# Optimization experiments

Measured on AMD Instinct MI355X. Metric: run time of the kernel, lower is better.

## Reference

```python
import jax, jax.numpy as jnp
import numpy as np
from jax import lax

V = 100000       # vocab_size / num_words
E = 300          # embedding_size (== num_units, required by compare stage)
M = 300          # num_units / mem_dim
NC = 3           # num_classes
L = 128          # leaves per tree -> N = 2L-1 nodes
N = 2 * L - 1


def build_tree(num_leaves):
    # balanced binary tree, postorder node numbering (children before parent)
    left, right = [], []
    def rec(lo, hi):
        if hi - lo == 1:
            left.append(-1); right.append(-1)
            return len(left) - 1
        mid = (lo + hi) // 2
        l = rec(lo, mid)
        r = rec(mid, hi)
        left.append(l); right.append(r)
        return len(left) - 1
    rec(0, num_leaves)
    return np.asarray(left, np.int32), np.asarray(right, np.int32)


def setup_inputs() -> dict:
    key = jax.random.key(0)
    ks = jax.random.split(key, 20)
    l1, r1 = build_tree(L)
    l2, r2 = build_tree(L)
    s = 0.1  # param scale (stands in for orthogonal init)
    inp = {
        "sent1": jax.random.randint(ks[0], (N,), 0, V),
        "sent2": jax.random.randint(ks[1], (N,), 0, V),
        "left1": jnp.asarray(l1), "right1": jnp.asarray(r1),
        "left2": jnp.asarray(l2), "right2": jnp.asarray(r2),
        "emb": jax.random.normal(ks[2], (V, E), jnp.float32),
        # composer x-projections, gate order: [cx, ix, fx, ox]
        "Wx_i": jax.random.normal(ks[3], (4, M, E), jnp.float32) * s,
        "bx_i": jnp.zeros((4, M), jnp.float32),
        # composer h-projections, gate order: [u, i, lf, rf, o]
        "Wl_i": jax.random.normal(ks[4], (5, M, M), jnp.float32) * s,
        "Wr_i": jax.random.normal(ks[5], (5, M, M), jnp.float32) * s,
        "Wx_c": jax.random.normal(ks[6], (4, M, M), jnp.float32) * s,
        "bx_c": jnp.zeros((4, M), jnp.float32),
        "Wl_c": jax.random.normal(ks[7], (5, M, M), jnp.float32) * s,
        "Wr_c": jax.random.normal(ks[8], (5, M, M), jnp.float32) * s,
        "Wc": jax.random.normal(ks[9], (M, 4 * M), jnp.float32) * 0.01,
        "bc": jnp.zeros((M,), jnp.float32),
        "Wa1": jax.random.normal(ks[10], (M, 4 * M), jnp.float32) * 0.01,
        "ba1": jnp.zeros((M,), jnp.float32),
        "Wa2": jax.random.normal(ks[11], (NC, M), jnp.float32) * 0.01,
        "ba2": jnp.zeros((NC,), jnp.float32),
    }
    return inp


def tree_lstm(xg, left, right, Wl, Wr):
    # xg: [N, 4, M] precomputed x-gate terms (cx, ix, fx, ox)
    # Wl/Wr: [5, M, M] hidden-state gate weights (u, i, lf, rf, o)
    n, _, m = xg.shape
    zero = jnp.zeros((m,), xg.dtype)

    def step(carry, t):
        C, H = carry
        i, l, r = t
        lc = jnp.where(l >= 0, C[jnp.maximum(l, 0)], zero)
        lh = jnp.where(l >= 0, H[jnp.maximum(l, 0)], zero)
        rc = jnp.where(r >= 0, C[jnp.maximum(r, 0)], zero)
        rh = jnp.where(r >= 0, H[jnp.maximum(r, 0)], zero)
        gl = jnp.einsum('gmd,d->gm', Wl, lh)  # [5, M]
        gr = jnp.einsum('gmd,d->gm', Wr, rh)
        x = xg[i]  # [4, M]
        u  = jnp.tanh(x[0] + gl[0] + gr[0])
        ig = jax.nn.sigmoid(x[1] + gl[1] + gr[1])
        lf = jax.nn.sigmoid(x[2] + gl[2] + gr[2])  # fx shared for both forgets (as in source)
        rf = jax.nn.sigmoid(x[2] + gl[3] + gr[3])
        c = ig * u + lf * lc + rf * rc
        o = jax.nn.sigmoid(x[3] + gl[4] + gr[4])
        h = o * jnp.tanh(c)
        return (C.at[i].set(c), H.at[i].set(h)), None

    init = (jnp.zeros((n, m), xg.dtype), jnp.zeros((n, m), xg.dtype))
    (_, H), _ = lax.scan(step, init, (jnp.arange(n), left, right))
    return H  # [N, M] all node hidden states in postorder


def reference(sent1, sent2, left1, right1, left2, right2, emb,
              Wx_i, bx_i, Wl_i, Wr_i, Wx_c, bx_c, Wl_c, Wr_c,
              Wc, bc, Wa1, ba1, Wa2, ba2):
    pad = emb.shape[0] - 1  # num_words - 1

    def encode(sent, left, right):
        # leaves embed their token; internal nodes embed PAD (PAD=True path)
        tok = jnp.where(left < 0, sent, pad)
        x = emb[tok]                                        # [N, E]
        xg = jnp.einsum('nd,gmd->ngm', x, Wx_i) + bx_i      # [N, 4, M]
        return tree_lstm(xg, left, right, Wl_i, Wr_i)

    s1 = encode(sent1, left1, right1)  # [N1, M]
    s2 = encode(sent2, left2, right2)  # [N2, M]

    raw = s1 @ s2.T                                         # [N1, N2]
    beta = jax.nn.softmax(raw, axis=1) @ s2                 # aligned to s1
    alpha = jax.nn.softmax(raw.T, axis=1) @ s1              # aligned to s2

    def compare(s, a, left, right):
        feat = jnp.concatenate([s, a, s - a, s * a], axis=-1)  # [N, 4M]
        h = jax.nn.relu(feat @ Wc.T + bc)                      # [N, M]
        xg = jnp.einsum('nd,gmd->ngm', h, Wx_c) + bx_c
        return tree_lstm(xg, left, right, Wl_c, Wr_c)

    v1 = compare(s1, beta, left1, right1)
    v2 = compare(s2, alpha, left2, right2)

    agg = jnp.concatenate([v1.mean(0), v1.max(0), v2.mean(0), v2.max(0)])  # [4M]
    hidden = jax.nn.relu(agg @ Wa1.T + ba1)
    logits = hidden @ Wa2.T + ba2
    return logits[None, :]  # [1, num_classes]
```

## Files before the change

### kernel.cpp

```cpp
#include <hip/hip_runtime.h>
#include <math.h>

#define NN 255
#define TC 510
#define HTLD 512
#define RSH 5

typedef unsigned int uint32;

__device__ __forceinline__ float sigm(float x){ return 1.f/(1.f+expf(-x)); }

__device__ __forceinline__ float aload(const float* p){ return __hip_atomic_load(p, __ATOMIC_RELAXED, __HIP_MEMORY_SCOPE_AGENT); }
__device__ __forceinline__ void astore(float* p, float v){ __hip_atomic_store(p, v, __ATOMIC_RELAXED, __HIP_MEMORY_SCOPE_AGENT); }
__device__ __forceinline__ uint32 aloadu(const uint32* p){ return __hip_atomic_load(p, __ATOMIC_RELAXED, __HIP_MEMORY_SCOPE_AGENT); }

__device__ __forceinline__ void leaf_gate(const float* __restrict__ xgp, int m, float& c, float& h){
  float x0 = xgp[m], x1 = xgp[300+m], x3 = xgp[900+m];
  float u = tanhf(x0), ig = sigm(x1);
  c = ig * u;
  h = sigm(x3) * tanhf(c);
}

__global__ __launch_bounds__(512) void k_setup(const int* __restrict__ l1, const int* __restrict__ r1,
                                               const int* __restrict__ l2, const int* __restrict__ r2,
                                               int4* __restrict__ lists2, int* __restrict__ cnt)
{
  __shared__ int lv[TC];
  __shared__ int cs[16];
  int t = threadIdx.x;
  if (t < TC) lv[t] = 0;
  if (t < 16) cs[t] = 0;
  __syncthreads();
  for (int it = 0; it < 12; ++it){
    int nv = 0;
    if (t < TC){
      int tr = t >= NN, i = t - tr * NN;
      const int* L = tr ? l2 : l1;
      const int* R = tr ? r2 : r1;
      int l = L[i], r = R[i];
      nv = (l < 0) ? 0 : 1 + max(lv[tr * NN + l], lv[tr * NN + r]);
    }
    __syncthreads();
    if (t < TC) lv[t] = nv;
    __syncthreads();
  }
  if (t < TC){
    int tr = t >= NN, i = t - tr * NN;
    int v = min(lv[t], 15);
    int pos = atomicAdd(&cs[v], 1);
    int l = (tr ? l2 : l1)[i], r = (tr ? r2 : r1)[i];
    lists2[v * 256 + pos] = make_int4(tr * NN + i, tr * NN + max(l, 0), tr * NN + max(r, 0), 0);
  }
  __syncthreads();
  if (t < 16) cnt[t] = cs[t];
}

template<int NG>
__global__ __launch_bounds__(256, 3) void k_tree(
    const float* __restrict__ Wl, const float* __restrict__ Wr,
    const float* __restrict__ xg, int xrow,
    float* __restrict__ H, float* __restrict__ C, float* __restrict__ HT,
    const int4* __restrict__ lists2, const int* __restrict__ cnt,
    uint32* __restrict__ rdy)
{
  constexpr int NB = NG * 75;
  __shared__ float Hs[16][2][320];
  __shared__ float Cs[16][4][2];
  __shared__ float Xs[16][4][4];
  __shared__ int4 nfo[512];
  __shared__ int lvoff[9];

  const int tid = threadIdx.x;
  const int lane = tid & 63, team = tid >> 6;
  const int mblk = blockIdx.x % 75, grp = blockIdx.x / 75;
  const int m = mblk * 4 + team;

  float wl[5][5], wr[5][5];
  #pragma unroll
  for (int g = 0; g < 5; ++g)
    #pragma unroll
    for (int j = 0; j < 5; ++j){
      int d = j * 64 + lane;
      size_t o = ((size_t)g * 300 + m) * 300 + d;
      wl[g][j] = (d < 300) ? Wl[o] : 0.f;
      wr[g][j] = (d < 300) ? Wr[o] : 0.f;
    }

  if (tid == 0){ lvoff[0] = 0; for (int lv = 1; lv <= 7; ++lv) lvoff[lv] = lvoff[lv-1] + cnt[lv-1]; }
  __syncthreads();
  for (int lv = 0; lv <= 7; ++lv)
    for (int i = tid; i < cnt[lv]; i += 256)
      nfo[lvoff[lv] + i] = lists2[lv * 256 + i];
  __syncthreads();

  {
    int nodes = cnt[0];
    int npg = (nodes + NG - 1) / NG;
    int n0 = grp * npg, n1 = min(nodes, n0 + npg);
    for (int nb0 = n0; nb0 < n1; nb0 += 64){
      int nch = min(64, n1 - nb0);
      if (tid < nch * 4){
        int ni = tid >> 2, tm = tid & 3;
        int gi = nfo[nb0 + ni].x;
        int mm = mblk * 4 + tm;
        float c, h; leaf_gate(xg + (size_t)gi * 1200, mm, c, h);
        astore(&C[(size_t)gi * 300 + mm], c);
        astore(&H[(size_t)gi * 300 + mm], h);
        astore(&HT[(size_t)mm * HTLD + gi], h);
      }
      asm volatile("s_waitcnt vmcnt(0)" ::: "memory");
      __syncthreads();
      if (tid < nch) atomicAdd(&rdy[(uint32)nfo[nb0 + tid].x << RSH], 1u);
    }
  }

  for (int lv = 1; lv <= 7; ++lv){
    int nodes = cnt[lv];
    int npg = (nodes + NG - 1) / NG;
    int n0 = grp * npg, n1 = min(nodes, n0 + npg);
    for (int nb0 = n0; nb0 < n1; nb0 += 16){
      int nch = min(16, n1 - nb0);
      int base = lvoff[lv] + nb0;
      __syncthreads();
      if (tid < nch){
        int4 nn = nfo[base + tid];
        while (aloadu(&rdy[(uint32)nn.y << RSH]) < 75u) __builtin_amdgcn_s_sleep(4);
        while (aloadu(&rdy[(uint32)nn.z << RSH]) < 75u) __builtin_amdgcn_s_sleep(4);
      }
      __syncthreads();
      #pragma unroll
      for (int p = 0; p < 2; ++p){
        int niA = team + p * 8, niB = niA + 4;
        bool vA = niA < nch, vB = niB < nch;
        int4 na = vA ? nfo[base + niA] : make_int4(0, 0, 0, 0);
        int4 nb4 = vB ? nfo[base + niB] : make_int4(0, 0, 0, 0);
        int d0 = lane, d1 = 64 + lane, d2 = 128 + lane, d3 = 192 + lane, d4 = 256 + lane;
        bool i4 = d4 < 300;
        #define LDH(ci, dd, ok) ((ok) ? aload(&H[(size_t)(ci) * 300 + (dd)]) : 0.f)
        float a0=LDH(na.y,d0,vA), a1=LDH(na.y,d1,vA), a2=LDH(na.y,d2,vA), a3=LDH(na.y,d3,vA), a4=LDH(na.y,d4,vA&&i4);
        float a5=LDH(na.z,d0,vA), a6=LDH(na.z,d1,vA), a7=LDH(na.z,d2,vA), a8=LDH(na.z,d3,vA), a9=LDH(na.z,d4,vA&&i4);
        float c0=LDH(nb4.y,d0,vB), c1=LDH(nb4.y,d1,vB), c2=LDH(nb4.y,d2,vB), c3=LDH(nb4.y,d3,vB), c4=LDH(nb4.y,d4,vB&&i4);
        float c5=LDH(nb4.z,d0,vB), c6=LDH(nb4.z,d1,vB), c7=LDH(nb4.z,d2,vB), c8=LDH(nb4.z,d3,vB), c9=LDH(nb4.z,d4,vB&&i4);
        #undef LDH
        if (vA){
          Hs[niA][0][d0]=a0; Hs[niA][0][d1]=a1; Hs[niA][0][d2]=a2; Hs[niA][0][d3]=a3; Hs[niA][0][d4]=a4;
          Hs[niA][1][d0]=a5; Hs[niA][1][d1]=a6; Hs[niA][1][d2]=a7; Hs[niA][1][d3]=a8; Hs[niA][1][d4]=a9;
        }
        if (vB){
          Hs[niB][0][d0]=c0; Hs[niB][0][d1]=c1; Hs[niB][0][d2]=c2; Hs[niB][0][d3]=c3; Hs[niB][0][d4]=c4;
          Hs[niB][1][d0]=c5; Hs[niB][1][d1]=c6; Hs[niB][1][d2]=c7; Hs[niB][1][d3]=c8; Hs[niB][1][d4]=c9;
        }
      }
      if (tid < 128){
        int ni = tid >> 3, tm = (tid >> 1) & 3, side = tid & 1;
        if (ni < nch){
          int4 nn = nfo[base + ni];
          int child = side ? nn.z : nn.y;
          Cs[ni][tm][side] = aload(&C[(size_t)child * 300 + mblk * 4 + tm]);
        }
      }
      {
        int ni = tid >> 4, tm = (tid >> 2) & 3, g = tid & 3;
        if (ni < nch){
          int row = (xrow >= 0) ? xrow : nfo[base + ni].x;
          Xs[ni][tm][g] = xg[(size_t)row * 1200 + g * 300 + mblk * 4 + tm];
        }
      }
      __syncthreads();
      #pragma unroll 2
      for (int ni = 0; ni < nch; ++ni){
        float p0 = 0.f, p1 = 0.f, p2 = 0.f, p3 = 0.f, p4 = 0.f;
        #pragma unroll
        for (int j = 0; j < 5; ++j){
          float hl = Hs[ni][0][j * 64 + lane];
          float hr = Hs[ni][1][j * 64 + lane];
          p0 += wl[0][j] * hl + wr[0][j] * hr;
          p1 += wl[1][j] * hl + wr[1][j] * hr;
          p2 += wl[2][j] * hl + wr[2][j] * hr;
          p3 += wl[3][j] * hl + wr[3][j] * hr;
          p4 += wl[4][j] * hl + wr[4][j] * hr;
        }
        #pragma unroll
        for (int off = 32; off; off >>= 1){
          p0 += __shfl_xor(p0, off); p1 += __shfl_xor(p1, off); p2 += __shfl_xor(p2, off);
          p3 += __shfl_xor(p3, off); p4 += __shfl_xor(p4, off);
        }
        if (lane == 0){
          int4 nn = nfo[base + ni];
          int gi = nn.x;
          float lc = Cs[ni][team][0], rc = Cs[ni][team][1];
          float u  = tanhf(Xs[ni][team][0] + p0);
          float ig = sigm (Xs[ni][team][1] + p1);
          float lf = sigm (Xs[ni][team][2] + p2);
          float rf = sigm (Xs[ni][team][2] + p3);
          float o  = sigm (Xs[ni][team][3] + p4);
          float cc = ig * u + lf * lc + rf * rc;
          float hv = o * tanhf(cc);
          astore(&C[(size_t)gi * 300 + m], cc);
          astore(&H[(size_t)gi * 300 + m], hv);
          astore(&HT[(size_t)m * HTLD + gi], hv);
        }
      }
      asm volatile("s_waitcnt vmcnt(0)" ::: "memory");
      __syncthreads();
      if (tid < nch) atomicAdd(&rdy[(uint32)nfo[base + tid].x << RSH], 1u);
    }
  }
}

__global__ __launch_bounds__(256) void k_xg(const int* __restrict__ sent1, const int* __restrict__ sent2,
                                            const int* __restrict__ l1, const int* __restrict__ l2,
                                            const float* __restrict__ emb, int pad,
                                            const float* __restrict__ W, const float* __restrict__ bias,
                                            const float* __restrict__ hsrc, float* __restrict__ out)
{
  __shared__ float Z[8][300];
  __shared__ int wr_s[8];
  int tx = threadIdx.x, ty = threadIdx.y;
  int t = ty * 64 + tx;
  int colbase = blockIdx.y * 8;
  if (t < 8){
    int gcol = colbase + t;
    int w = 0;
    if (hsrc) w = (gcol < TC) ? 1 : 0;
    else {
      if (gcol == TC) w = 1;
      else if (gcol < TC){
        int tr = gcol >= NN, node = gcol - tr * NN;
        w = ((tr ? l2 : l1)[node] < 0) ? 1 : 0;
      }
    }
    wr_s[t] = w;
  }
  __syncthreads();
  for (int c = 0; c < 8; ++c){
    int gcol = colbase + c;
    if (wr_s[c]){
      if (hsrc){
        for (int k = t; k < 300; k += 256) Z[c][k] = hsrc[(size_t)gcol * 300 + k];
      } else {
        int tok;
        if (gcol == TC) tok = pad;
        else { int tr = gcol >= NN; tok = (tr ? sent2 : sent1)[gcol - tr * NN]; }
        const float* e = emb + (size_t)tok * 300;
        for (int k = t; k < 300; k += 256) Z[c][k] = e[k];
      }
    } else {
      for (int k = t; k < 300; k += 256) Z[c][k] = 0.f;
    }
  }
  __syncthreads();
  int r = blockIdx.x * 64 + tx;
  if (r < 1200){
    float a0 = 0.f, a1 = 0.f;
    const float* wp = W + (size_t)r * 300;
    for (int k = 0; k < 300; k += 4){
      float4 wv = *(const float4*)(wp + k);
      float4 z0 = *(const float4*)(&Z[ty][k]);
      float4 z1 = *(const float4*)(&Z[ty + 4][k]);
      a0 += wv.x*z0.x + wv.y*z0.y + wv.z*z0.z + wv.w*z0.w;
      a1 += wv.x*z1.x + wv.y*z1.y + wv.z*z1.z + wv.w*z1.w;
    }
    float b = bias[r];
    int g0 = colbase + ty, g1 = colbase + ty + 4;
    if (g0 <= TC && wr_s[ty])     out[(size_t)g0 * 1200 + r] = a0 + b;
    if (g1 <= TC && wr_s[ty + 4]) out[(size_t)g1 * 1200 + r] = a1 + b;
  }
}

__global__ __launch_bounds__(256) void k_attn2(const float* __restrict__ H, const float* __restrict__ HT,
                                               float* __restrict__ ab)
{
  __shared__ float q[4][304];
  __shared__ float S[4][256];
  __shared__ float red[256];
  __shared__ float invs[4];
  int t = threadIdx.x;
  int dir = blockIdx.x >= 64;
  int r0 = (blockIdx.x - dir * 64) * 4;
  int nr = min(4, NN - r0);
  const float* Ss = H + (dir ? (size_t)NN * 300 : 0);
  const float* So = H + (dir ? 0 : (size_t)NN * 300);
  int oppb = dir ? 0 : NN;

  for (int idx = t; idx < 4 * 304; idx += 256){
    int r = idx / 304, k = idx - r * 304;
    q[r][k] = (r < nr && k < 300) ? Ss[(size_t)(r0 + r) * 300 + k] : 0.f;
  }
  __syncthreads();

  float s0 = 0.f, s1 = 0.f, s2 = 0.f, s3 = 0.f;
  if (t < NN){
    const float* hp = HT + oppb + t;
    #pragma unroll 4
    for (int k = 0; k < 300; ++k){
      float ht = hp[(size_t)k * HTLD];
      s0 += q[0][k] * ht; s1 += q[1][k] * ht; s2 += q[2][k] * ht; s3 += q[3][k] * ht;
    }
  }
  S[0][t] = (t < NN) ? s0 : -1e30f;
  S[1][t] = (t < NN) ? s1 : -1e30f;
  S[2][t] = (t < NN) ? s2 : -1e30f;
  S[3][t] = (t < NN) ? s3 : -1e30f;
  __syncthreads();

  for (int r = 0; r < nr; ++r){
    red[t] = S[r][t];
    __syncthreads();
    for (int s = 128; s; s >>= 1){ if (t < s) red[t] = fmaxf(red[t], red[t + s]); __syncthreads(); }
    float mx = red[0];
    __syncthreads();
    float e = (t < NN) ? expf(S[r][t] - mx) : 0.f;
    S[r][t] = e;
    red[t] = e;
    __syncthreads();
    for (int s = 128; s; s >>= 1){ if (t < s) red[t] += red[t + s]; __syncthreads(); }
    if (t == 0) invs[r] = 1.f / red[0];
    __syncthreads();
  }

  float a0=0,a1=0,a2=0,a3=0, b0=0,b1=0,b2=0,b3=0;
  int m2 = t + 256;
  bool has2 = m2 < 300;
  for (int j = 0; j < NN; ++j){
    const float* sp = So + (size_t)j * 300;
    float v1 = (t < 300) ? sp[t] : 0.f;
    float v2 = has2 ? sp[m2] : 0.f;
    float p0 = S[0][j], p1 = S[1][j], p2 = S[2][j], p3 = S[3][j];
    a0 += p0 * v1; a1 += p1 * v1; a2 += p2 * v1; a3 += p3 * v1;
    b0 += p0 * v2; b1 += p1 * v2; b2 += p2 * v2; b3 += p3 * v2;
  }
  float accs1[4] = {a0, a1, a2, a3};
  float accs2[4] = {b0, b1, b2, b3};
  for (int r = 0; r < nr; ++r){
    size_t rowo = (size_t)(dir * NN + r0 + r) * 300;
    if (t < 300) ab[rowo + t] = accs1[r] * invs[r];
    if (has2)    ab[rowo + m2] = accs2[r] * invs[r];
  }
}

__global__ __launch_bounds__(256) void k_hcmp(const float* __restrict__ Henc, const float* __restrict__ ab,
                                              const float* __restrict__ Wc, const float* __restrict__ bc,
                                              float* __restrict__ hc)
{
  __shared__ float Z[8][1200];
  int tx = threadIdx.x, ty = threadIdx.y;
  int t = ty * 64 + tx;
  int colbase = blockIdx.y * 8;
  for (int c = 0; c < 8; ++c){
    int gcol = colbase + c;
    if (gcol < TC){
      const float* sp = Henc + (size_t)gcol * 300;
      const float* ap = ab + (size_t)gcol * 300;
      for (int k = t; k < 1200; k += 256){
        int sel = k >= 900 ? 3 : (k >= 600 ? 2 : (k >= 300 ? 1 : 0));
        int kk = k - sel * 300;
        float s = sp[kk], a = ap[kk];
        Z[c][k] = sel == 0 ? s : sel == 1 ? a : sel == 2 ? (s - a) : (s * a);
      }
    } else {
      for (int k = t; k < 1200; k += 256) Z[c][k] = 0.f;
    }
  }
  __syncthreads();
  int r = blockIdx.x * 64 + tx;
  if (r < 300){
    float a0 = 0.f, a1 = 0.f;
    const float* wp = Wc + (size_t)r * 1200;
    for (int k = 0; k < 1200; k += 4){
      float4 wv = *(const float4*)(wp + k);
      float4 z0 = *(const float4*)(&Z[ty][k]);
      float4 z1 = *(const float4*)(&Z[ty + 4][k]);
      a0 += wv.x*z0.x + wv.y*z0.y + wv.z*z0.z + wv.w*z0.w;
      a1 += wv.x*z1.x + wv.y*z1.y + wv.z*z1.z + wv.w*z1.w;
    }
    float b = bc[r];
    int g0 = colbase + ty, g1 = colbase + ty + 4;
    if (g0 < TC) hc[(size_t)g0 * 300 + r] = fmaxf(a0 + b, 0.f);
    if (g1 < TC) hc[(size_t)g1 * 300 + r] = fmaxf(a1 + b, 0.f);
  }
}

__global__ __launch_bounds__(256) void k_agg(const float* __restrict__ HTc, float* __restrict__ agg)
{
  __shared__ float red[256];
  int idx = blockIdx.x;
  int tr = idx / 300, m = idx - tr * 300;
  int t = threadIdx.x;
  const float* p = HTc + (size_t)m * HTLD + tr * NN;
  float v = (t < NN) ? p[t] : 0.f;
  red[t] = v;
  __syncthreads();
  for (int s = 128; s; s >>= 1){ if (t < s) red[t] += red[t + s]; __syncthreads(); }
  float sum = red[0];
  __syncthreads();
  red[t] = (t < NN) ? v : -1e30f;
  __syncthreads();
  for (int s = 128; s; s >>= 1){ if (t < s) red[t] = fmaxf(red[t], red[t + s]); __syncthreads(); }
  if (t == 0){
    agg[tr * 600 + m] = sum / 255.f;
    agg[tr * 600 + 300 + m] = red[0];
  }
}

__global__ __launch_bounds__(256) void k_mlp1(const float* __restrict__ agg,
                                              const float* __restrict__ Wa1, const float* __restrict__ ba1,
                                              float* __restrict__ hid)
{
  __shared__ float red[256];
  int h = blockIdx.x, t = threadIdx.x;
  const float* wp = Wa1 + (size_t)h * 1200;
  float a = 0.f;
  for (int k = t; k < 1200; k += 256) a += wp[k] * agg[k];
  red[t] = a;
  __syncthreads();
  for (int s = 128; s; s >>= 1){ if (t < s) red[t] += red[t + s]; __syncthreads(); }
  if (t == 0) hid[h] = fmaxf(red[0] + ba1[h], 0.f);
}

__global__ __launch_bounds__(256) void k_mlp2(const float* __restrict__ hid,
                                              const float* __restrict__ Wa2, const float* __restrict__ ba2,
                                              float* __restrict__ out)
{
  __shared__ float h_s[300];
  int t = threadIdx.x;
  for (int k = t; k < 300; k += 256) h_s[k] = hid[k];
  __syncthreads();
  if (t < 192){
    int c = t >> 6, ln = t & 63;
    float a = 0.f;
    for (int k = ln; k < 300; k += 64) a += Wa2[c * 300 + k] * h_s[k];
    #pragma unroll
    for (int off = 32; off; off >>= 1) a += __shfl_down(a, off);
    if (ln == 0) out[c] = a + ba2[c];
  }
}

extern "C" void kernel_launch(void* const* d_in, const int* in_sizes, int n_in,
                              void* d_out, int out_size, void* d_ws, size_t ws_size,
                              hipStream_t stream)
{
  const int*   sent1 = (const int*)d_in[0];
  const int*   sent2 = (const int*)d_in[1];
  const int*   l1    = (const int*)d_in[2];
  const int*   r1    = (const int*)d_in[3];
  const int*   l2    = (const int*)d_in[4];
  const int*   r2    = (const int*)d_in[5];
  const float* emb   = (const float*)d_in[6];
  const float* Wx_i  = (const float*)d_in[7];
  const float* bx_i  = (const float*)d_in[8];
  const float* Wl_i  = (const float*)d_in[9];
  const float* Wr_i  = (const float*)d_in[10];
  const float* Wx_c  = (const float*)d_in[11];
  const float* bx_c  = (const float*)d_in[12];
  const float* Wl_c  = (const float*)d_in[13];
  const float* Wr_c  = (const float*)d_in[14];
  const float* Wcm   = (const float*)d_in[15];
  const float* bcm   = (const float*)d_in[16];
  const float* Wa1   = (const float*)d_in[17];
  const float* ba1   = (const float*)d_in[18];
  const float* Wa2   = (const float*)d_in[19];
  const float* ba2   = (const float*)d_in[20];
  int V = in_sizes[6] / 300;
  int pad = V - 1;

  char* w = (char*)d_ws;
  uint32* rdy1   = (uint32*)w;
  uint32* rdy2   = (uint32*)(w + 65536);
  int*    cnt    = (int*)(w + 131072);
  int4*   lists2 = (int4*)(w + 131136);
  float* xg   = (float*)(w + 131136 + 65536);
  float* Henc = xg + 613200;
  float* Hcmp = Henc + 153000;
  float* C    = Hcmp + 153000;
  float* ab   = C + 153000;
  float* hc   = ab + 153000;
  float* HTe  = hc + 153000;
  float* HTc  = HTe + 153600;
  float* agg  = HTc + 153600;
  float* hid  = agg + 1200;
  float* outp = (float*)d_out;

  hipMemsetAsync(rdy1, 0, 131072, stream);

  int nb6 = 0, nCU = 0;
  hipError_t eq = hipOccupancyMaxActiveBlocksPerMultiprocessor(&nb6, reinterpret_cast<const void*>(&k_tree<8>), 256, 0);
  hipError_t ec = hipDeviceGetAttribute(&nCU, hipDeviceAttributeMultiprocessorCount, 0);
  bool ok600 = (eq == hipSuccess) && (ec == hipSuccess) && (nb6 * nCU >= 600);

  k_setup<<<1, 512, 0, stream>>>(l1, r1, l2, r2, lists2, cnt);
  dim3 blk(64, 4);
  int padRow = TC;
  int ownRow = -1;

  k_xg<<<dim3(19, 64), blk, 0, stream>>>(sent1, sent2, l1, l2, emb, pad, Wx_i, bx_i, nullptr, xg);
  {
    void* args[] = {(void*)&Wl_i, (void*)&Wr_i, (void*)&xg, (void*)&padRow,
                    (void*)&Henc, (void*)&C, (void*)&HTe, (void*)&lists2, (void*)&cnt, (void*)&rdy1};
    if (ok600) hipLaunchCooperativeKernel((void*)&k_tree<8>, dim3(600), dim3(256), args, 0, stream);
    else       hipLaunchCooperativeKernel((void*)&k_tree<4>, dim3(300), dim3(256), args, 0, stream);
  }

  k_attn2<<<128, 256, 0, stream>>>(Henc, HTe, ab);

  k_hcmp<<<dim3(5, 64), blk, 0, stream>>>(Henc, ab, Wcm, bcm, hc);
  k_xg<<<dim3(19, 64), blk, 0, stream>>>(sent1, sent2, l1, l2, emb, pad, Wx_c, bx_c, hc, xg);
  {
    void* args[] = {(void*)&Wl_c, (void*)&Wr_c, (void*)&xg, (void*)&ownRow,
                    (void*)&Hcmp, (void*)&C, (void*)&HTc, (void*)&lists2, (void*)&cnt, (void*)&rdy2};
    if (ok600) hipLaunchCooperativeKernel((void*)&k_tree<8>, dim3(600), dim3(256), args, 0, stream);
    else       hipLaunchCooperativeKernel((void*)&k_tree<4>, dim3(300), dim3(256), args, 0, stream);
  }

  k_agg<<<600, 256, 0, stream>>>(HTc, agg);
  k_mlp1<<<300, 256, 0, stream>>>(agg, Wa1, ba1, hid);
  k_mlp2<<<1, 256, 0, stream>>>(hid, Wa2, ba2, outp);
}
```

Measured before the change: 490.1 us.

## Remap tree blocks per XCD and widen column tiles in projection kernels

The tree kernel now launches 640 blocks and maps block IDs so that each M-block's groups share the same XCD (blockIdx & 7). Blocks with an out-of-range mblk exit early. This is meant to keep the cross-block readiness flags and shared H/C traffic within one XCD's L2. The k_xg and k_hcmp matvec kernels now process 32 and 16 node columns per block instead of 8, which reuses each weight load across more columns and cuts redundant weight reads. The trade-off is more registers and LDS per block, and the tree kernel now needs 640 resident blocks for the fast path.

After: 491.2 us. No clear change (+0.2%).

```diff
diff --git a/kernel.cpp b/kernel.cpp
--- a/kernel.cpp
+++ b/kernel.cpp
@@ -55,7 +55,7 @@
   if (t < 16) cnt[t] = cs[t];
 }
 
-template<int NG>
+template<int NG, int REMAP>
 __global__ __launch_bounds__(256, 3) void k_tree(
     const float* __restrict__ Wl, const float* __restrict__ Wr,
     const float* __restrict__ xg, int xrow,
@@ -63,16 +63,26 @@
     const int4* __restrict__ lists2, const int* __restrict__ cnt,
     uint32* __restrict__ rdy)
 {
-  constexpr int NB = NG * 75;
   __shared__ float Hs[16][2][320];
   __shared__ float Cs[16][4][2];
   __shared__ float Xs[16][4][4];
   __shared__ int4 nfo[512];
   __shared__ int lvoff[9];
 
+  int mblk, grp;
+  if (REMAP){
+    int xcd = blockIdx.x & 7;
+    int i   = blockIdx.x >> 3;
+    mblk = xcd + 8 * (i % 10);
+    grp  = i / 10;
+    if (mblk >= 75) return;
+  } else {
+    mblk = blockIdx.x % 75;
+    grp  = blockIdx.x / 75;
+  }
+
   const int tid = threadIdx.x;
   const int lane = tid & 63, team = tid >> 6;
-  const int mblk = blockIdx.x % 75, grp = blockIdx.x / 75;
   const int m = mblk * 4 + team;
 
   float wl[5][5], wr[5][5];
@@ -208,18 +218,18 @@
   }
 }
 
-__global__ __launch_bounds__(256) void k_xg(const int* __restrict__ sent1, const int* __restrict__ sent2,
-                                            const int* __restrict__ l1, const int* __restrict__ l2,
-                                            const float* __restrict__ emb, int pad,
-                                            const float* __restrict__ W, const float* __restrict__ bias,
-                                            const float* __restrict__ hsrc, float* __restrict__ out)
-{
-  __shared__ float Z[8][300];
-  __shared__ int wr_s[8];
+__global__ __launch_bounds__(256) void k_xgw(const int* __restrict__ sent1, const int* __restrict__ sent2,
+                                             const int* __restrict__ l1, const int* __restrict__ l2,
+                                             const float* __restrict__ emb, int pad,
+                                             const float* __restrict__ W, const float* __restrict__ bias,
+                                             const float* __restrict__ hsrc, float* __restrict__ out)
+{
+  __shared__ float Z[32][304];
+  __shared__ int wr_s[32];
   int tx = threadIdx.x, ty = threadIdx.y;
   int t = ty * 64 + tx;
-  int colbase = blockIdx.y * 8;
-  if (t < 8){
+  int colbase = blockIdx.y * 32;
+  if (t < 32){
     int gcol = colbase + t;
     int w = 0;
     if (hsrc) w = (gcol < TC) ? 1 : 0;
@@ -233,38 +243,40 @@
     wr_s[t] = w;
   }
   __syncthreads();
-  for (int c = 0; c < 8; ++c){
+  for (int idx = t; idx < 32 * 300; idx += 256){
+    int c = idx / 300, d = idx - c * 300;
     int gcol = colbase + c;
+    float v = 0.f;
     if (wr_s[c]){
-      if (hsrc){
-        for (int k = t; k < 300; k += 256) Z[c][k] = hsrc[(size_t)gcol * 300 + k];
-      } else {
+      if (hsrc) v = hsrc[(size_t)gcol * 300 + d];
+      else {
         int tok;
         if (gcol == TC) tok = pad;
         else { int tr = gcol >= NN; tok = (tr ? sent2 : sent1)[gcol - tr * NN]; }
-        const float* e = emb + (size_t)tok * 300;
-        for (int k = t; k < 300; k += 256) Z[c][k] = e[k];
-      }
-    } else {
-      for (int k = t; k < 300; k += 256) Z[c][k] = 0.f;
-    }
+        v = emb[(size_t)tok * 300 + d];
+      }
+    }
+    Z[c][d] = v;
   }
   __syncthreads();
   int r = blockIdx.x * 64 + tx;
-  if (r < 1200){
-    float a0 = 0.f, a1 = 0.f;
-    const float* wp = W + (size_t)r * 300;
-    for (int k = 0; k < 300; k += 4){
-      float4 wv = *(const float4*)(wp + k);
-      float4 z0 = *(const float4*)(&Z[ty][k]);
-      float4 z1 = *(const float4*)(&Z[ty + 4][k]);
-      a0 += wv.x*z0.x + wv.y*z0.y + wv.z*z0.z + wv.w*z0.w;
-      a1 += wv.x*z1.x + wv.y*z1.y + wv.z*z1.z + wv.w*z1.w;
-    }
-    float b = bias[r];
-    int g0 = colbase + ty, g1 = colbase + ty + 4;
-    if (g0 <= TC && wr_s[ty])     out[(size_t)g0 * 1200 + r] = a0 + b;
-    if (g1 <= TC && wr_s[ty + 4]) out[(size_t)g1 * 1200 + r] = a1 + b;
+  if (r >= 1200) return;
+  float acc[8] = {0.f,0.f,0.f,0.f,0.f,0.f,0.f,0.f};
+  const float* wp = W + (size_t)r * 300;
+  for (int k = 0; k < 300; k += 4){
+    float4 wv = *(const float4*)(wp + k);
+    #pragma unroll
+    for (int cc = 0; cc < 8; ++cc){
+      float4 z = *(const float4*)(&Z[ty * 8 + cc][k]);
+      acc[cc] += wv.x*z.x + wv.y*z.y + wv.z*z.z + wv.w*z.w;
+    }
+  }
+  float b = bias[r];
+  #pragma unroll
+  for (int cc = 0; cc < 8; ++cc){
+    int c = ty * 8 + cc;
+    int gcol = colbase + c;
+    if (gcol <= TC && wr_s[c]) out[(size_t)gcol * 1200 + r] = acc[cc] + b;
   }
 }
 
@@ -339,45 +351,44 @@
   }
 }
 
-__global__ __launch_bounds__(256) void k_hcmp(const float* __restrict__ Henc, const float* __restrict__ ab,
-                                              const float* __restrict__ Wc, const float* __restrict__ bc,
-                                              float* __restrict__ hc)
-{
-  __shared__ float Z[8][1200];
+__global__ __launch_bounds__(256, 2) void k_hcmpw(const float* __restrict__ Henc, const float* __restrict__ ab,
+                                                  const float* __restrict__ Wc, const float* __restrict__ bc,
+                                                  float* __restrict__ hc)
+{
+  __shared__ float Z[16][1200];
   int tx = threadIdx.x, ty = threadIdx.y;
   int t = ty * 64 + tx;
-  int colbase = blockIdx.y * 8;
-  for (int c = 0; c < 8; ++c){
+  int colbase = blockIdx.y * 16;
+  for (int idx = t; idx < 16 * 1200; idx += 256){
+    int c = idx / 1200, rem = idx - c * 1200;
     int gcol = colbase + c;
+    float v = 0.f;
     if (gcol < TC){
-      const float* sp = Henc + (size_t)gcol * 300;
-      const float* ap = ab + (size_t)gcol * 300;
-      for (int k = t; k < 1200; k += 256){
-        int sel = k >= 900 ? 3 : (k >= 600 ? 2 : (k >= 300 ? 1 : 0));
-        int kk = k - sel * 300;
-        float s = sp[kk], a = ap[kk];
-        Z[c][k] = sel == 0 ? s : sel == 1 ? a : sel == 2 ? (s - a) : (s * a);
-      }
-    } else {
-      for (int k = t; k < 1200; k += 256) Z[c][k] = 0.f;
-    }
+      int sel = rem >= 900 ? 3 : rem >= 600 ? 2 : rem >= 300 ? 1 : 0;
+      int kk = rem - sel * 300;
+      float s = Henc[(size_t)gcol * 300 + kk], a = ab[(size_t)gcol * 300 + kk];
+      v = sel == 0 ? s : sel == 1 ? a : sel == 2 ? (s - a) : (s * a);
+    }
+    Z[c][rem] = v;
   }
   __syncthreads();
   int r = blockIdx.x * 64 + tx;
-  if (r < 300){
-    float a0 = 0.f, a1 = 0.f;
-    const float* wp = Wc + (size_t)r * 1200;
-    for (int k = 0; k < 1200; k += 4){
-      float4 wv = *(const float4*)(wp + k);
-      float4 z0 = *(const float4*)(&Z[ty][k]);
-      float4 z1 = *(const float4*)(&Z[ty + 4][k]);
-      a0 += wv.x*z0.x + wv.y*z0.y + wv.z*z0.z + wv.w*z0.w;
-      a1 += wv.x*z1.x + wv.y*z1.y + wv.z*z1.z + wv.w*z1.w;
-    }
-    float b = bc[r];
-    int g0 = colbase + ty, g1 = colbase + ty + 4;
-    if (g0 < TC) hc[(size_t)g0 * 300 + r] = fmaxf(a0 + b, 0.f);
-    if (g1 < TC) hc[(size_t)g1 * 300 + r] = fmaxf(a1 + b, 0.f);
+  if (r >= 300) return;
+  float acc[4] = {0.f, 0.f, 0.f, 0.f};
+  const float* wp = Wc + (size_t)r * 1200;
+  for (int k = 0; k < 1200; k += 4){
+    float4 wv = *(const float4*)(wp + k);
+    #pragma unroll
+    for (int cc = 0; cc < 4; ++cc){
+      float4 z = *(const float4*)(&Z[ty * 4 + cc][k]);
+      acc[cc] += wv.x*z.x + wv.y*z.y + wv.z*z.z + wv.w*z.w;
+    }
+  }
+  float b = bc[r];
+  #pragma unroll
+  for (int cc = 0; cc < 4; ++cc){
+    int gcol = colbase + ty * 4 + cc;
+    if (gcol < TC) hc[(size_t)gcol * 300 + r] = fmaxf(acc[cc] + b, 0.f);
   }
 }
 
@@ -484,32 +495,32 @@
   hipMemsetAsync(rdy1, 0, 131072, stream);
 
   int nb6 = 0, nCU = 0;
-  hipError_t eq = hipOccupancyMaxActiveBlocksPerMultiprocessor(&nb6, reinterpret_cast<const void*>(&k_tree<8>), 256, 0);
+  hipError_t eq = hipOccupancyMaxActiveBlocksPerMultiprocessor(&nb6, reinterpret_cast<const void*>(&k_tree<8, 1>), 256, 0);
   hipError_t ec = hipDeviceGetAttribute(&nCU, hipDeviceAttributeMultiprocessorCount, 0);
-  bool ok600 = (eq == hipSuccess) && (ec == hipSuccess) && (nb6 * nCU >= 600);
+  bool ok640 = (eq == hipSuccess) && (ec == hipSuccess) && (nb6 * nCU >= 640);
 
   k_setup<<<1, 512, 0, stream>>>(l1, r1, l2, r2, lists2, cnt);
   dim3 blk(64, 4);
   int padRow = TC;
   int ownRow = -1;
 
-  k_xg<<<dim3(19, 64), blk, 0, stream>>>(sent1, sent2, l1, l2, emb, pad, Wx_i, bx_i, nullptr, xg);
+  k_xgw<<<dim3(19, 16), blk, 0, stream>>>(sent1, sent2, l1, l2, emb, pad, Wx_i, bx_i, nullptr, xg);
   {
     void* args[] = {(void*)&Wl_i, (void*)&Wr_i, (void*)&xg, (void*)&padRow,
                     (void*)&Henc, (void*)&C, (void*)&HTe, (void*)&lists2, (void*)&cnt, (void*)&rdy1};
-    if (ok600) hipLaunchCooperativeKernel((void*)&k_tree<8>, dim3(600), dim3(256), args, 0, stream);
-    else       hipLaunchCooperativeKernel((void*)&k_tree<4>, dim3(300), dim3(256), args, 0, stream);
+    if (ok640) hipLaunchCooperativeKernel((void*)&k_tree<8, 1>, dim3(640), dim3(256), args, 0, stream);
+    else       hipLaunchCooperativeKernel((void*)&k_tree<4, 0>, dim3(300), dim3(256), args, 0, stream);
   }
 
   k_attn2<<<128, 256, 0, stream>>>(Henc, HTe, ab);
 
-  k_hcmp<<<dim3(5, 64), blk, 0, stream>>>(Henc, ab, Wcm, bcm, hc);
-  k_xg<<<dim3(19, 64), blk, 0, stream>>>(sent1, sent2, l1, l2, emb, pad, Wx_c, bx_c, hc, xg);
+  k_hcmpw<<<dim3(5, 32), blk, 0, stream>>>(Henc, ab, Wcm, bcm, hc);
+  k_xgw<<<dim3(19, 16), blk, 0, stream>>>(sent1, sent2, l1, l2, emb, pad, Wx_c, bx_c, hc, xg);
   {
     void* args[] = {(void*)&Wl_c, (void*)&Wr_c, (void*)&xg, (void*)&ownRow,
                     (void*)&Hcmp, (void*)&C, (void*)&HTc, (void*)&lists2, (void*)&cnt, (void*)&rdy2};
-    if (ok600) hipLaunchCooperativeKernel((void*)&k_tree<8>, dim3(600), dim3(256), args, 0, stream);
-    else       hipLaunchCooperativeKernel((void*)&k_tree<4>, dim3(300), dim3(256), args, 0, stream);
+    if (ok640) hipLaunchCooperativeKernel((void*)&k_tree<8, 1>, dim3(640), dim3(256), args, 0, stream);
+    else       hipLaunchCooperativeKernel((void*)&k_tree<4, 0>, dim3(300), dim3(256), args, 0, stream);
   }
 
   k_agg<<<600, 256, 0, stream>>>(HTc, agg);
```
